# Optimization experiments

Measured on AMD Instinct MI355X. Metric: run time of the kernel, lower is better.

Reference implementation:

```python
import jax, jax.numpy as jnp
import numpy as np

EPS = 1e-6
TEMP_GEO = 0.07
W_LOCAL = 0.5
W_SHARP = 0.5


def _l2norm(x):
    return x / jnp.clip(jnp.linalg.norm(x, axis=-1, keepdims=True), 1e-12)


def setup_inputs() -> dict:
    key = jax.random.key(0)
    ks = jax.random.split(key, 6)
    B, L, S, C = 8, 1024, 1024, 128
    N, P = 8, 256
    q_geo = _l2norm(jax.random.normal(ks[0], (B, L, C), jnp.float32))
    geo_pos = _l2norm(jax.random.normal(ks[1], (B, S, C), jnp.float32))
    label = jax.random.randint(ks[2], (B, L, S), 0, 2, jnp.int32)
    q_cl = jax.random.normal(ks[3], (N, P, C), jnp.float32)
    cl_pos = jax.random.normal(ks[4], (N, P, C), jnp.float32)
    idx = jax.random.randint(ks[5], (N,), 0, P, jnp.int32)
    return {"q_geo": q_geo, "q_cl": q_cl, "geo_pos": geo_pos,
            "cl_pos": cl_pos, "label": label, "idx": idx}


def _masked_mean(v, m):
    # per-sample mean over the [L,S] plane of entries where m is True
    m = m.astype(v.dtype)
    return jnp.sum(v * m, axis=(1, 2)) / jnp.maximum(jnp.sum(m, axis=(1, 2)), 1.0)


def _loftr_loss(conf, label):
    # standard LoFTR coarse CE loss (LoFTRLoss source absent from repo snippet)
    conf = jnp.clip(conf, EPS, 1.0 - EPS)
    pos = label == 1
    neg = label == 0
    pos_loss = _masked_mean(-jnp.log(conf), pos)          # [B]
    neg_loss = _masked_mean(-jnp.log(1.0 - conf), neg)    # [B]
    loss = pos_loss + neg_loss
    return jnp.mean(loss), jnp.mean(pos_loss), jnp.mean(neg_loss)


def _geometric_loss(q, k, label):
    sim = jnp.einsum('blc,bsc->bls', q, k) / TEMP_GEO        # [B,L,S]
    conf = jax.nn.softmax(sim, axis=1) * jax.nn.softmax(sim, axis=2)
    return _loftr_loss(conf, label)


def _sharpness_loss(q, k, label):
    sim = (1.0 + jnp.einsum('blc,bsc->bls', q, k)) / 2.0     # [B,L,S]
    # column stats (over L, dim=0 per sample) -> sharpness1 [B,S]
    s1 = (jnp.max(sim, axis=1) - jnp.mean(sim, axis=1)) / jnp.std(sim, axis=1, ddof=1)
    sharp1 = jax.nn.softmax(s1, axis=-1)
    # row stats (over S, dim=1 per sample) -> sharpness2 [B,L]
    s2 = (jnp.max(sim, axis=2) - jnp.mean(sim, axis=2)) / jnp.std(sim, axis=2, ddof=1)
    sharp2 = jax.nn.softmax(s2, axis=-1)
    simc = jnp.clip(sim, EPS, 1.0 - EPS)
    nll = -jnp.log(simc)
    pos = (label == 1).astype(simc.dtype)
    neg = (label == 0)
    loss1 = jnp.sum(nll * sharp1[:, None, :] * pos, axis=(1, 2))   # [B]
    loss2 = jnp.sum(nll * sharp2[:, :, None] * pos, axis=(1, 2))   # [B]
    loss3 = _masked_mean(-jnp.log(1.0 - simc), neg)                # [B]
    losses = (loss1 + loss2) / 2.0 + loss3
    return sharp1, jnp.mean(losses)


def _contrast_loss(q, all_k):
    # intended math of GeCoContrast: full cosine matrix, diag positives, tail negatives
    N = q.shape[0]
    sim = (1.0 + _l2norm(q) @ _l2norm(all_k).T) / 2.0   # [N, M]
    sim = jnp.clip(sim, EPS, 1.0 - EPS)
    l_pos = jnp.diagonal(sim[:, :N])                    # [N]
    l_neg = sim[:, N:]                                  # [N, M-N]
    return (jnp.mean(-jnp.log(l_pos)) + jnp.mean(-jnp.log(1.0 - l_neg))) / 2.0


def _forward(q_geo, q_cl, geo_pos, cl_pos, label, idx):
    loss_geo, geo_pos_loss, geo_neg_loss = _geometric_loss(q_geo, geo_pos, label)
    sharpness, loss_sharp = _sharpness_loss(q_geo, geo_pos, label)
    loss_geo = ((1.0 - W_SHARP) * loss_geo + W_SHARP * loss_sharp) * W_LOCAL

    N, P, C = q_cl.shape
    ar = jnp.arange(N)
    q_sel = q_cl[ar, idx]                               # [N,C]
    sel = cl_pos[ar, idx]                               # [N,C] positives moved to slot 0
    first = cl_pos[:, 0, :]
    swapped = cl_pos.at[ar, idx].set(first).at[:, 0, :].set(sel)
    cl_pos_save = sel
    all_k = jnp.concatenate([swapped[:, 0, :],
                             swapped[:, 1:, :].reshape(N * (P - 1), C)], axis=0)
    loss_cl = _contrast_loss(q_sel, all_k) * (1.0 - W_LOCAL)

    total = loss_geo + loss_cl
    return (sharpness, cl_pos_save, total, geo_pos_loss, geo_neg_loss, loss_sharp, loss_cl)


def reference(q_geo, q_cl, geo_pos, cl_pos, label, idx):
    return _forward(q_geo, q_cl, geo_pos, cl_pos, label, idx)
```

## Files before the change

### kernel.cpp

```cpp
#include <hip/hip_runtime.h>
#include <math.h>

#define BB 8
#define LL 1024
#define SS 1024
#define CC 128
#define NN 8
#define PP 256

static constexpr float EPS       = 1e-6f;
static constexpr float ONE_M_EPS = 1.0f - 1e-6f;
static constexpr float INV_T     = 1.0f / 0.07f;
static constexpr float NLL_MAX   = 13.815511f;
static constexpr float NLL_MIN   = 1.0000005e-6f;

static constexpr size_t DOTSZ      = (size_t)BB * LL * SS;
static constexpr size_t OFF_LSER   = DOTSZ;
static constexpr size_t OFF_LSEC   = DOTSZ + 16384;
static constexpr size_t OFF_SHARP2 = DOTSZ + 32768;
static constexpr size_t OFF_RP     = DOTSZ + 40960;
static constexpr size_t OFF_CP     = OFF_RP + 524288;
static constexpr size_t OFF_ACC    = OFF_CP + 524288;
static constexpr size_t OFF_ACCCL  = OFF_ACC + 48;
static constexpr size_t OFF_QN     = OFF_ACC + 64;

static constexpr int OUT_CLSAVE = 8192;
static constexpr int OUT_SCAL   = 9216;

typedef __bf16 bf16x8 __attribute__((ext_vector_type(8)));
typedef float  floatx4 __attribute__((ext_vector_type(4)));

__device__ __forceinline__ void split_f4(float4 x,
                                         unsigned& hp0, unsigned& hp1,
                                         unsigned& lp0, unsigned& lp1) {
    unsigned u0 = __builtin_bit_cast(unsigned, x.x);
    unsigned u1 = __builtin_bit_cast(unsigned, x.y);
    unsigned u2 = __builtin_bit_cast(unsigned, x.z);
    unsigned u3 = __builtin_bit_cast(unsigned, x.w);
    unsigned r0 = u0 + 0x7FFFu + ((u0 >> 16) & 1u);
    unsigned r1 = u1 + 0x7FFFu + ((u1 >> 16) & 1u);
    unsigned r2 = u2 + 0x7FFFu + ((u2 >> 16) & 1u);
    unsigned r3 = u3 + 0x7FFFu + ((u3 >> 16) & 1u);
    float s0 = x.x - __builtin_bit_cast(float, r0 & 0xFFFF0000u);
    float s1 = x.y - __builtin_bit_cast(float, r1 & 0xFFFF0000u);
    float s2 = x.z - __builtin_bit_cast(float, r2 & 0xFFFF0000u);
    float s3 = x.w - __builtin_bit_cast(float, r3 & 0xFFFF0000u);
    hp0 = __builtin_amdgcn_perm(r1, r0, 0x07060302u);
    hp1 = __builtin_amdgcn_perm(r3, r2, 0x07060302u);
    lp0 = __builtin_amdgcn_perm(__builtin_bit_cast(unsigned, s1),
                                __builtin_bit_cast(unsigned, s0), 0x07060302u);
    lp1 = __builtin_amdgcn_perm(__builtin_bit_cast(unsigned, s3),
                                __builtin_bit_cast(unsigned, s2), 0x07060302u);
}

__global__ __launch_bounds__(256, 2) void gemm_dot(const float* __restrict__ A,
                                                   const float* __restrict__ Bm,
                                                   const float* __restrict__ q_cl,
                                                   const float* __restrict__ cl_pos,
                                                   const int* __restrict__ idx,
                                                   float* __restrict__ out,
                                                   float* __restrict__ dot,
                                                   float* __restrict__ ws) {
    __shared__ __align__(16) char lds[2][32768];

    int tid  = threadIdx.x;
    int lane = tid & 63;
    int w    = tid >> 6;

    if (blockIdx.x == 512) {
        if (tid < 52) ws[OFF_ACC + tid] = 0.0f;
        for (int n = w; n < NN; n += 4) {
            int in = idx[n];
            const float* q = q_cl + ((size_t)(n * PP + in)) * CC;
            float2 qv = *(const float2*)(q + 2 * lane);
            float ss = qv.x * qv.x + qv.y * qv.y;
            for (int o = 32; o; o >>= 1) ss += __shfl_xor(ss, o);
            float inv = 1.0f / fmaxf(sqrtf(ss), 1e-12f);
            *(float2*)(ws + OFF_QN + n * 128 + 2 * lane) = make_float2(qv.x * inv, qv.y * inv);
            const float* cp = cl_pos + ((size_t)(n * PP + in)) * CC;
            float2 cv = *(const float2*)(cp + 2 * lane);
            *(float2*)(out + OUT_CLSAVE + n * 128 + 2 * lane) = cv;
        }
        return;
    }

    int t  = blockIdx.x;
    int b  = t >> 6;
    int rm = t & 63;
    int bl = rm >> 3, bs = rm & 7;
    int R0 = bl * 128, C0 = bs * 128;

    const float* Ab = A  + ((size_t)(b * 1024 + R0)) * CC;
    const float* Bb = Bm + ((size_t)(b * 1024 + C0)) * CC;

    const float* srcu[4];
    int hib[4], lob[4];
#pragma unroll
    for (int u = 0; u < 4; u++) {
        int g   = u * 256 + tid;
        int mat = g >> 9;
        int r   = (g >> 2) & 127;
        int c8  = g & 3;
        srcu[u] = (mat ? Bb : Ab) + (size_t)r * CC + c8 * 8;
        int base = mat * 16384 + r * 128;
        int sw   = r & 7;
        hib[u] = base + ((c8 ^ sw) * 16);
        lob[u] = base + (((c8 + 4) ^ sw) * 16);
    }

    int fl   = lane & 15;
    int quad = lane >> 4;
    int wr   = w >> 1, wc = w & 1;
    int Rw   = wr * 64, Cw = wc * 64;

    floatx4 acc[4][4];
#pragma unroll
    for (int i = 0; i < 4; i++)
#pragma unroll
        for (int j = 0; j < 4; j++) acc[i][j] = (floatx4){0.f, 0.f, 0.f, 0.f};

    float4 v0[4], v1[4];
#pragma unroll
    for (int u = 0; u < 4; u++) {
        v0[u] = *(const float4*)(srcu[u]);
        v1[u] = *(const float4*)(srcu[u] + 4);
    }
#pragma unroll
    for (int u = 0; u < 4; u++) {
        unsigned h0, h1, h2, h3, l0, l1, l2, l3;
        split_f4(v0[u], h0, h1, l0, l1);
        split_f4(v1[u], h2, h3, l2, l3);
        *(uint4*)(&lds[0][hib[u]]) = make_uint4(h0, h1, h2, h3);
        *(uint4*)(&lds[0][lob[u]]) = make_uint4(l0, l1, l2, l3);
    }
    __syncthreads();

    for (int ks = 0; ks < 4; ks++) {
        int cur = ks & 1;
        if (ks < 3) {
#pragma unroll
            for (int u = 0; u < 4; u++) {
                v0[u] = *(const float4*)(srcu[u] + (ks + 1) * 32);
                v1[u] = *(const float4*)(srcu[u] + (ks + 1) * 32 + 4);
            }
        }
        const char* la = lds[cur];
        const char* lb = lds[cur] + 16384;
        bf16x8 ah[4], al[4];
#pragma unroll
        for (int mt = 0; mt < 4; mt++) {
            int row = Rw + mt * 16 + fl;
            int sw  = row & 7;
            ah[mt] = *(const bf16x8*)(la + row * 128 + ((quad ^ sw) * 16));
            al[mt] = *(const bf16x8*)(la + row * 128 + (((quad + 4) ^ sw) * 16));
        }
#pragma unroll
        for (int nt = 0; nt < 4; nt++) {
            int row = Cw + nt * 16 + fl;
            int sw  = row & 7;
            bf16x8 bh  = *(const bf16x8*)(lb + row * 128 + ((quad ^ sw) * 16));
            bf16x8 blo = *(const bf16x8*)(lb + row * 128 + (((quad + 4) ^ sw) * 16));
#pragma unroll
            for (int mt = 0; mt < 4; mt++) {
                acc[mt][nt] = __builtin_amdgcn_mfma_f32_16x16x32_bf16(ah[mt], bh,  acc[mt][nt], 0, 0, 0);
                acc[mt][nt] = __builtin_amdgcn_mfma_f32_16x16x32_bf16(ah[mt], blo, acc[mt][nt], 0, 0, 0);
                acc[mt][nt] = __builtin_amdgcn_mfma_f32_16x16x32_bf16(al[mt], bh,  acc[mt][nt], 0, 0, 0);
            }
        }
        if (ks < 3) {
            char* nxt = lds[cur ^ 1];
#pragma unroll
            for (int u = 0; u < 4; u++) {
                unsigned h0, h1, h2, h3, l0, l1, l2, l3;
                split_f4(v0[u], h0, h1, l0, l1);
                split_f4(v1[u], h2, h3, l2, l3);
                *(uint4*)(&nxt[hib[u]]) = make_uint4(h0, h1, h2, h3);
                *(uint4*)(&nxt[lob[u]]) = make_uint4(l0, l1, l2, l3);
            }
        }
        __syncthreads();
    }

#pragma unroll
    for (int mt = 0; mt < 4; mt++)
#pragma unroll
        for (int nt = 0; nt < 4; nt++) {
            int col = C0 + Cw + nt * 16 + fl;
#pragma unroll
            for (int r = 0; r < 4; r++) {
                int row = R0 + Rw + mt * 16 + quad * 4 + r;
                dot[((size_t)(b * 1024 + row)) * 1024 + col] = acc[mt][nt][r];
            }
        }

    int stile = bs * 2 + wc;
    int ltile = bl * 2 + wr;
    float ces[4], cmx[4], csm[4], csq[4];
#pragma unroll
    for (int nt = 0; nt < 4; nt++) { ces[nt] = 0.f; cmx[nt] = -1e30f; csm[nt] = 0.f; csq[nt] = 0.f; }
#pragma unroll
    for (int mt = 0; mt < 4; mt++) {
#pragma unroll
        for (int r = 0; r < 4; r++) {
            float es = 0.f, mx = -1e30f, sm = 0.f, sq = 0.f;
#pragma unroll
            for (int nt = 0; nt < 4; nt++) {
                float d  = acc[mt][nt][r];
                float e  = __expf(d * INV_T);
                float s2 = fmaf(0.5f, d, 0.5f);
                es += e; mx = fmaxf(mx, s2); sm += s2; sq += s2 * s2;
                ces[nt] += e; cmx[nt] = fmaxf(cmx[nt], s2); csm[nt] += s2; csq[nt] += s2 * s2;
            }
            for (int o = 1; o < 16; o <<= 1) {
                es += __shfl_xor(es, o);
                mx = fmaxf(mx, __shfl_xor(mx, o));
                sm += __shfl_xor(sm, o);
                sq += __shfl_xor(sq, o);
            }
            if (fl == 0) {
                int row = R0 + Rw + mt * 16 + quad * 4 + r;
                *(float4*)(ws + OFF_RP + (((size_t)(b * 16 + stile)) * 1024 + row) * 4) =
                    make_float4(es, mx, sm, sq);
            }
        }
    }
#pragma unroll
    for (int nt = 0; nt < 4; nt++) {
        float es = ces[nt], mx = cmx[nt], sm = csm[nt], sq = csq[nt];
        for (int o = 16; o < 64; o <<= 1) {
            es += __shfl_xor(es, o);
            mx = fmaxf(mx, __shfl_xor(mx, o));
            sm += __shfl_xor(sm, o);
            sq += __shfl_xor(sq, o);
        }
        if (quad == 0) {
            int col = C0 + Cw + nt * 16 + fl;
            *(float4*)(ws + OFF_CP + (((size_t)(b * 16 + ltile)) * 1024 + col) * 4) =
                make_float4(es, mx, sm, sq);
        }
    }
}

__global__ __launch_bounds__(256) void mid(const float* __restrict__ cl_pos,
                                           const int* __restrict__ idx,
                                           float* __restrict__ ws,
                                           float* __restrict__ out) {
    int q   = blockIdx.x;
    int tid = threadIdx.x;
    int lane = tid & 63, wid = tid >> 6;

    if (q < 16) {
        bool docol = (q < 8);
        int b = q & 7;
        const float* part = ws + (docol ? OFF_CP : OFF_RP);
        float* lse = ws + (docol ? OFF_LSEC : OFF_LSER) + (size_t)b * 1024;
        float zs[4];
        float mxall = -1e30f;
#pragma unroll
        for (int r = 0; r < 4; r++) {
            int i = tid + r * 256;
            float es = 0.f, mx = -1e30f, sm = 0.f, sq = 0.f;
#pragma unroll
            for (int t = 0; t < 16; t++) {
                float4 v = *(const float4*)(part + (((size_t)(b * 16 + t)) * 1024 + i) * 4);
                es += v.x; mx = fmaxf(mx, v.y); sm += v.z; sq += v.w;
            }
            float mean = sm * (1.0f / 1024.0f);
            float var  = (sq - sm * sm * (1.0f / 1024.0f)) * (1.0f / 1023.0f);
            zs[r] = (mx - mean) / sqrtf(fmaxf(var, 1e-30f));
            mxall = fmaxf(mxall, zs[r]);
            lse[i] = __logf(es);
        }
        __shared__ float sb[4];
        __shared__ float red;
        float mx = mxall;
        for (int o = 32; o; o >>= 1) mx = fmaxf(mx, __shfl_xor(mx, o));
        if (!lane) sb[wid] = mx;
        __syncthreads();
        if (tid == 0) red = fmaxf(fmaxf(sb[0], sb[1]), fmaxf(sb[2], sb[3]));
        __syncthreads();
        mx = red;
        float e[4]; float smv = 0.f;
#pragma unroll
        for (int r = 0; r < 4; r++) { e[r] = __expf(zs[r] - mx); smv += e[r]; }
        for (int o = 32; o; o >>= 1) smv += __shfl_xor(smv, o);
        __syncthreads();
        if (!lane) sb[wid] = smv;
        __syncthreads();
        if (tid == 0) red = sb[0] + sb[1] + sb[2] + sb[3];
        __syncthreads();
        float inv = 1.0f / red;
        float* dst = docol ? (out + (size_t)b * 1024) : (ws + OFF_SHARP2 + (size_t)b * 1024);
#pragma unroll
        for (int r = 0; r < 4; r++) dst[tid + r * 256] = e[r] * inv;
    } else {
        int j = (q - 16) * 4 + wid;
        int m, p;
        if (j < NN) {
            m = j; p = idx[j];
        } else {
            int jj = j - NN;
            m = jj / (PP - 1);
            p = 1 + (jj - m * (PP - 1));
            if (p == idx[m]) p = 0;
        }
        const float* k = cl_pos + ((size_t)(m * PP + p)) * CC;
        float2 kv = *(const float2*)(k + 2 * lane);
        float ksq = kv.x * kv.x + kv.y * kv.y;
        for (int o = 32; o; o >>= 1) ksq += __shfl_xor(ksq, o);
        float invkn = 1.0f / fmaxf(sqrtf(ksq), 1e-12f);
        float pos = 0.0f, neg = 0.0f;
        if (j < NN) {
            const float2 qv = *(const float2*)(ws + OFF_QN + j * 128 + 2 * lane);
            float dt = qv.x * kv.x + qv.y * kv.y;
            for (int o = 32; o; o >>= 1) dt += __shfl_xor(dt, o);
            float sim = fminf(fmaxf(fmaf(0.5f * invkn, dt, 0.5f), EPS), ONE_M_EPS);
            pos = -__logf(sim);
        } else {
#pragma unroll
            for (int n = 0; n < NN; n++) {
                const float2 qv = *(const float2*)(ws + OFF_QN + n * 128 + 2 * lane);
                float dt = qv.x * kv.x + qv.y * kv.y;
                for (int o = 32; o; o >>= 1) dt += __shfl_xor(dt, o);
                float om = fminf(fmaxf(fmaf(-0.5f * invkn, dt, 0.5f), EPS), ONE_M_EPS);
                neg -= __logf(om);
            }
        }
        __shared__ float cb[2][4];
        if (!lane) { cb[0][wid] = pos; cb[1][wid] = neg; }
        __syncthreads();
        if (tid == 0) {
            float ps = cb[0][0] + cb[0][1] + cb[0][2] + cb[0][3];
            float ng = cb[1][0] + cb[1][1] + cb[1][2] + cb[1][3];
            if (ps != 0.0f) atomicAdd(ws + OFF_ACCCL + 0, ps);
            if (ng != 0.0f) atomicAdd(ws + OFF_ACCCL + 1, ng);
        }
    }
}

__device__ __forceinline__ void proc_elem(float d, int lab, float lcj, float sh1j,
                                          float lr, float s2v,
                                          float& posg, float& negg, float& l1, float& l2,
                                          float& negs, float& pcf) {
    float t = lr + lcj - d * (2.0f * INV_T);
    float isPos = (lab == 1) ? 1.0f : 0.0f;
    float isNeg = 1.0f - isPos;
    float tp   = fminf(fmaxf(t, NLL_MIN), NLL_MAX);
    float simc = fminf(fmaxf(fmaf(0.5f, d, 0.5f), EPS), ONE_M_EPS);
    float om   = fminf(fmaxf(fmaf(-0.5f, d, 0.5f), EPS), ONE_M_EPS);
    float nll2 = -__logf(simc);
    float cf   = fminf(fmaxf(__expf(-t), EPS), ONE_M_EPS);
    float nllg = -__logf(1.0f - cf);
    float nlls = -__logf(om);
    posg += isPos * tp;
    l1   += isPos * nll2 * sh1j;
    l2   += isPos * nll2 * s2v;
    pcf  += isPos;
    negg += isNeg * nllg;
    negs += isNeg * nlls;
}

__global__ __launch_bounds__(256) void main_loss(const float* __restrict__ dot,
                                                 const int* __restrict__ label,
                                                 const float* __restrict__ sharp1,
                                                 float* __restrict__ ws) {
    int b = blockIdx.y;
    int l0 = blockIdx.x * 4;
    int s = threadIdx.x * 4;
    float4 lc4 = *(const float4*)(ws + OFF_LSEC + (size_t)b * 1024 + s);
    float4 sh1 = *(const float4*)(sharp1 + (size_t)b * 1024 + s);
    const float* lser = ws + OFF_LSER + (size_t)b * 1024;
    const float* sh2  = ws + OFF_SHARP2 + (size_t)b * 1024;
    float posg = 0, negg = 0, l1 = 0, l2 = 0, negs = 0, pcf = 0;
#pragma unroll
    for (int r = 0; r < 4; r++) {
        int l = l0 + r;
        float lr  = lser[l];
        float s2v = sh2[l];
        size_t base = ((size_t)(b * 1024 + l)) * 1024 + s;
        float4 d4 = *(const float4*)(dot + base);
        int4  lb  = *(const int4*)(label + base);
        proc_elem(d4.x, lb.x, lc4.x, sh1.x, lr, s2v, posg, negg, l1, l2, negs, pcf);
        proc_elem(d4.y, lb.y, lc4.y, sh1.y, lr, s2v, posg, negg, l1, l2, negs, pcf);
        proc_elem(d4.z, lb.z, lc4.z, sh1.z, lr, s2v, posg, negg, l1, l2, negs, pcf);
        proc_elem(d4.w, lb.w, lc4.w, sh1.w, lr, s2v, posg, negg, l1, l2, negs, pcf);
    }
    float vals[6] = {posg, negg, l1, l2, negs, pcf};
    __shared__ float sb[6][4];
    int lane = threadIdx.x & 63, wid = threadIdx.x >> 6;
#pragma unroll
    for (int k = 0; k < 6; k++) {
        float v = vals[k];
        for (int o = 32; o; o >>= 1) v += __shfl_xor(v, o);
        if (!lane) sb[k][wid] = v;
    }
    __syncthreads();
    if (threadIdx.x < 6) {
        float r = sb[threadIdx.x][0] + sb[threadIdx.x][1] + sb[threadIdx.x][2] + sb[threadIdx.x][3];
        atomicAdd(ws + OFF_ACC + (size_t)b * 6 + threadIdx.x, r);
    }
}

__global__ void finalize(float* __restrict__ out, const float* __restrict__ ws) {
    if (threadIdx.x != 0) return;
    float gp = 0, gn = 0, lsh = 0;
    for (int b = 0; b < 8; b++) {
        const float* a = ws + OFF_ACC + (size_t)b * 6;
        float pc = a[5];
        float nc = (float)((size_t)LL * SS) - pc;
        gp += a[0] / fmaxf(pc, 1.0f);
        gn += a[1] / fmaxf(nc, 1.0f);
        lsh += (a[2] + a[3]) * 0.5f + a[4] / fmaxf(nc, 1.0f);
    }
    gp *= 0.125f; gn *= 0.125f; lsh *= 0.125f;
    float lgeo = gp + gn;
    float lgw = (0.5f * lgeo + 0.5f * lsh) * 0.5f;
    float clp = ws[OFF_ACCCL + 0] / 8.0f;
    float cln = ws[OFF_ACCCL + 1] / (8.0f * 2040.0f);
    float lcl = (clp + cln) * 0.5f * 0.5f;
    out[OUT_SCAL + 0] = lgw + lcl;
    out[OUT_SCAL + 1] = gp;
    out[OUT_SCAL + 2] = gn;
    out[OUT_SCAL + 3] = lsh;
    out[OUT_SCAL + 4] = lcl;
}

extern "C" void kernel_launch(void* const* d_in, const int* in_sizes, int n_in,
                              void* d_out, int out_size, void* d_ws, size_t ws_size,
                              hipStream_t stream) {
    const float* q_geo   = (const float*)d_in[0];
    const float* q_cl    = (const float*)d_in[1];
    const float* geo_pos = (const float*)d_in[2];
    const float* cl_pos  = (const float*)d_in[3];
    const int*   label   = (const int*)d_in[4];
    const int*   idx     = (const int*)d_in[5];
    float* out = (float*)d_out;
    float* ws  = (float*)d_ws;
    float* dot = ws;

    gemm_dot<<<dim3(513), dim3(256), 0, stream>>>(q_geo, geo_pos, q_cl, cl_pos, idx, out, dot, ws);
    mid<<<dim3(528), dim3(256), 0, stream>>>(cl_pos, idx, ws, out);
    main_loss<<<dim3(256, 8), dim3(256), 0, stream>>>(dot, label, out, ws);
    finalize<<<dim3(1), dim3(64), 0, stream>>>(out, ws);
}
```

Measured before the change: 148.6 us.

## Use 512-thread GEMM blocks and halve transcendental logs in loss elementwise

The GEMM kernel now runs 8 waves per 128x128 tile instead of 4, with each wave covering a 64x32 sub-tile. This doubles the number of row-partial stat slices, so the workspace layout and the mid-stage reduction loop are widened to match. In the per-element loss, positive and negative labels are mutually exclusive, so the two log calls are selected by the label and only two logs are evaluated instead of three. More waves per tile may hide more latency but raise synchronisation and partial-reduction traffic.

```diff
diff --git a/kernel.cpp b/kernel.cpp
--- a/kernel.cpp
+++ b/kernel.cpp
@@ -19,7 +19,7 @@
 static constexpr size_t OFF_LSEC   = DOTSZ + 16384;
 static constexpr size_t OFF_SHARP2 = DOTSZ + 32768;
 static constexpr size_t OFF_RP     = DOTSZ + 40960;
-static constexpr size_t OFF_CP     = OFF_RP + 524288;
+static constexpr size_t OFF_CP     = OFF_RP + 1048576;
 static constexpr size_t OFF_ACC    = OFF_CP + 524288;
 static constexpr size_t OFF_ACCCL  = OFF_ACC + 48;
 static constexpr size_t OFF_QN     = OFF_ACC + 64;
@@ -53,14 +53,14 @@
                                 __builtin_bit_cast(unsigned, s2), 0x07060302u);
 }
 
-__global__ __launch_bounds__(256, 2) void gemm_dot(const float* __restrict__ A,
-                                                   const float* __restrict__ Bm,
-                                                   const float* __restrict__ q_cl,
-                                                   const float* __restrict__ cl_pos,
-                                                   const int* __restrict__ idx,
-                                                   float* __restrict__ out,
-                                                   float* __restrict__ dot,
-                                                   float* __restrict__ ws) {
+__global__ __launch_bounds__(512) void gemm_dot(const float* __restrict__ A,
+                                                const float* __restrict__ Bm,
+                                                const float* __restrict__ q_cl,
+                                                const float* __restrict__ cl_pos,
+                                                const int* __restrict__ idx,
+                                                float* __restrict__ out,
+                                                float* __restrict__ dot,
+                                                float* __restrict__ ws) {
     __shared__ __align__(16) char lds[2][32768];
 
     int tid  = threadIdx.x;
@@ -69,7 +69,8 @@
 
     if (blockIdx.x == 512) {
         if (tid < 52) ws[OFF_ACC + tid] = 0.0f;
-        for (int n = w; n < NN; n += 4) {
+        int n = w;
+        if (n < NN) {
             int in = idx[n];
             const float* q = q_cl + ((size_t)(n * PP + in)) * CC;
             float2 qv = *(const float2*)(q + 2 * lane);
@@ -93,11 +94,11 @@
     const float* Ab = A  + ((size_t)(b * 1024 + R0)) * CC;
     const float* Bb = Bm + ((size_t)(b * 1024 + C0)) * CC;
 
-    const float* srcu[4];
-    int hib[4], lob[4];
-#pragma unroll
-    for (int u = 0; u < 4; u++) {
-        int g   = u * 256 + tid;
+    const float* srcu[2];
+    int hib[2], lob[2];
+#pragma unroll
+    for (int u = 0; u < 2; u++) {
+        int g   = u * 512 + tid;
         int mat = g >> 9;
         int r   = (g >> 2) & 127;
         int c8  = g & 3;
@@ -110,23 +111,23 @@
 
     int fl   = lane & 15;
     int quad = lane >> 4;
-    int wr   = w >> 1, wc = w & 1;
-    int Rw   = wr * 64, Cw = wc * 64;
-
-    floatx4 acc[4][4];
+    int wr   = w >> 2, wc = w & 3;
+    int Rw   = wr * 64, Cw = wc * 32;
+
+    floatx4 acc[4][2];
 #pragma unroll
     for (int i = 0; i < 4; i++)
 #pragma unroll
-        for (int j = 0; j < 4; j++) acc[i][j] = (floatx4){0.f, 0.f, 0.f, 0.f};
-
-    float4 v0[4], v1[4];
-#pragma unroll
-    for (int u = 0; u < 4; u++) {
+        for (int j = 0; j < 2; j++) acc[i][j] = (floatx4){0.f, 0.f, 0.f, 0.f};
+
+    float4 v0[2], v1[2];
+#pragma unroll
+    for (int u = 0; u < 2; u++) {
         v0[u] = *(const float4*)(srcu[u]);
         v1[u] = *(const float4*)(srcu[u] + 4);
     }
 #pragma unroll
-    for (int u = 0; u < 4; u++) {
+    for (int u = 0; u < 2; u++) {
         unsigned h0, h1, h2, h3, l0, l1, l2, l3;
         split_f4(v0[u], h0, h1, l0, l1);
         split_f4(v1[u], h2, h3, l2, l3);
@@ -139,7 +140,7 @@
         int cur = ks & 1;
         if (ks < 3) {
 #pragma unroll
-            for (int u = 0; u < 4; u++) {
+            for (int u = 0; u < 2; u++) {
                 v0[u] = *(const float4*)(srcu[u] + (ks + 1) * 32);
                 v1[u] = *(const float4*)(srcu[u] + (ks + 1) * 32 + 4);
             }
@@ -155,7 +156,7 @@
             al[mt] = *(const bf16x8*)(la + row * 128 + (((quad + 4) ^ sw) * 16));
         }
 #pragma unroll
-        for (int nt = 0; nt < 4; nt++) {
+        for (int nt = 0; nt < 2; nt++) {
             int row = Cw + nt * 16 + fl;
             int sw  = row & 7;
             bf16x8 bh  = *(const bf16x8*)(lb + row * 128 + ((quad ^ sw) * 16));
@@ -170,7 +171,7 @@
         if (ks < 3) {
             char* nxt = lds[cur ^ 1];
 #pragma unroll
-            for (int u = 0; u < 4; u++) {
+            for (int u = 0; u < 2; u++) {
                 unsigned h0, h1, h2, h3, l0, l1, l2, l3;
                 split_f4(v0[u], h0, h1, l0, l1);
                 split_f4(v1[u], h2, h3, l2, l3);
@@ -184,7 +185,7 @@
 #pragma unroll
     for (int mt = 0; mt < 4; mt++)
 #pragma unroll
-        for (int nt = 0; nt < 4; nt++) {
+        for (int nt = 0; nt < 2; nt++) {
             int col = C0 + Cw + nt * 16 + fl;
 #pragma unroll
             for (int r = 0; r < 4; r++) {
@@ -193,18 +194,18 @@
             }
         }
 
-    int stile = bs * 2 + wc;
+    int stile = bs * 4 + wc;
     int ltile = bl * 2 + wr;
-    float ces[4], cmx[4], csm[4], csq[4];
-#pragma unroll
-    for (int nt = 0; nt < 4; nt++) { ces[nt] = 0.f; cmx[nt] = -1e30f; csm[nt] = 0.f; csq[nt] = 0.f; }
+    float ces[2], cmx[2], csm[2], csq[2];
+#pragma unroll
+    for (int nt = 0; nt < 2; nt++) { ces[nt] = 0.f; cmx[nt] = -1e30f; csm[nt] = 0.f; csq[nt] = 0.f; }
 #pragma unroll
     for (int mt = 0; mt < 4; mt++) {
 #pragma unroll
         for (int r = 0; r < 4; r++) {
             float es = 0.f, mx = -1e30f, sm = 0.f, sq = 0.f;
 #pragma unroll
-            for (int nt = 0; nt < 4; nt++) {
+            for (int nt = 0; nt < 2; nt++) {
                 float d  = acc[mt][nt][r];
                 float e  = __expf(d * INV_T);
                 float s2 = fmaf(0.5f, d, 0.5f);
@@ -219,13 +220,13 @@
             }
             if (fl == 0) {
                 int row = R0 + Rw + mt * 16 + quad * 4 + r;
-                *(float4*)(ws + OFF_RP + (((size_t)(b * 16 + stile)) * 1024 + row) * 4) =
+                *(float4*)(ws + OFF_RP + (((size_t)(b * 32 + stile)) * 1024 + row) * 4) =
                     make_float4(es, mx, sm, sq);
             }
         }
     }
 #pragma unroll
-    for (int nt = 0; nt < 4; nt++) {
+    for (int nt = 0; nt < 2; nt++) {
         float es = ces[nt], mx = cmx[nt], sm = csm[nt], sq = csq[nt];
         for (int o = 16; o < 64; o <<= 1) {
             es += __shfl_xor(es, o);
@@ -252,7 +253,9 @@
     if (q < 16) {
         bool docol = (q < 8);
         int b = q & 7;
-        const float* part = ws + (docol ? OFF_CP : OFF_RP);
+        int TT = docol ? 16 : 32;
+        const float* pb = ws + (docol ? (OFF_CP + (size_t)b * 16 * 1024 * 4)
+                                      : (OFF_RP + (size_t)b * 32 * 1024 * 4));
         float* lse = ws + (docol ? OFF_LSEC : OFF_LSER) + (size_t)b * 1024;
         float zs[4];
         float mxall = -1e30f;
@@ -260,9 +263,8 @@
         for (int r = 0; r < 4; r++) {
             int i = tid + r * 256;
             float es = 0.f, mx = -1e30f, sm = 0.f, sq = 0.f;
-#pragma unroll
-            for (int t = 0; t < 16; t++) {
-                float4 v = *(const float4*)(part + (((size_t)(b * 16 + t)) * 1024 + i) * 4);
+            for (int t = 0; t < TT; t++) {
+                float4 v = *(const float4*)(pb + ((size_t)t * 1024 + i) * 4);
                 es += v.x; mx = fmaxf(mx, v.y); sm += v.z; sq += v.w;
             }
             float mean = sm * (1.0f / 1024.0f);
@@ -343,21 +345,23 @@
                                           float& posg, float& negg, float& l1, float& l2,
                                           float& negs, float& pcf) {
     float t = lr + lcj - d * (2.0f * INV_T);
-    float isPos = (lab == 1) ? 1.0f : 0.0f;
+    bool  pos   = (lab == 1);
+    float isPos = pos ? 1.0f : 0.0f;
     float isNeg = 1.0f - isPos;
     float tp   = fminf(fmaxf(t, NLL_MIN), NLL_MAX);
     float simc = fminf(fmaxf(fmaf(0.5f, d, 0.5f), EPS), ONE_M_EPS);
     float om   = fminf(fmaxf(fmaf(-0.5f, d, 0.5f), EPS), ONE_M_EPS);
-    float nll2 = -__logf(simc);
+    float x    = pos ? simc : om;
+    float nllx = -__logf(x);
     float cf   = fminf(fmaxf(__expf(-t), EPS), ONE_M_EPS);
-    float nllg = -__logf(1.0f - cf);
-    float nlls = -__logf(om);
+    float wi   = pos ? 1.0f : (1.0f - cf);
+    float nllw = -__logf(wi);
     posg += isPos * tp;
-    l1   += isPos * nll2 * sh1j;
-    l2   += isPos * nll2 * s2v;
+    l1   += isPos * nllx * sh1j;
+    l2   += isPos * nllx * s2v;
     pcf  += isPos;
-    negg += isNeg * nllg;
-    negs += isNeg * nlls;
+    negg += isNeg * nllw;
+    negs += isNeg * nllx;
 }
 
 __global__ __launch_bounds__(256) void main_loss(const float* __restrict__ dot,
@@ -438,7 +442,7 @@
     float* ws  = (float*)d_ws;
     float* dot = ws;
 
-    gemm_dot<<<dim3(513), dim3(256), 0, stream>>>(q_geo, geo_pos, q_cl, cl_pos, idx, out, dot, ws);
+    gemm_dot<<<dim3(513), dim3(512), 0, stream>>>(q_geo, geo_pos, q_cl, cl_pos, idx, out, dot, ws);
     mid<<<dim3(528), dim3(256), 0, stream>>>(cl_pos, idx, ws, out);
     main_loss<<<dim3(256, 8), dim3(256), 0, stream>>>(dot, label, out, ws);
     finalize<<<dim3(1), dim3(64), 0, stream>>>(out, ws);
```

After: 176.2 us. 1.19x slower.
